# Performance work log

Measured on AMD Instinct MI355X. Metric: run time of the kernel, lower is better.

Reference implementation:

```python
import jax, jax.numpy as jnp
import numpy as np

D_MODEL = 1024
N_HEADS = 16
D_FF = 4096
EPS = 1e-5


def setup_inputs() -> dict:
    key = jax.random.key(0)
    ks = jax.random.split(key, 10)
    sig_attn = (1.0 / D_MODEL) ** 0.5
    sig1 = (2.0 / (D_MODEL + D_FF)) ** 0.5
    sig2 = (2.0 / (D_FF + D_MODEL)) ** 0.5
    return {
        "x": jax.random.normal(ks[0], (4, 2048, D_MODEL), dtype=jnp.float32),
        "W_q": jax.random.normal(ks[1], (D_MODEL, D_MODEL), jnp.float32) * sig_attn,
        "W_k": jax.random.normal(ks[2], (D_MODEL, D_MODEL), jnp.float32) * sig_attn,
        "W_v": jax.random.normal(ks[3], (D_MODEL, D_MODEL), jnp.float32) * sig_attn,
        "W_o": jax.random.normal(ks[4], (D_MODEL, D_MODEL), jnp.float32) * sig_attn,
        "gamma1": jnp.ones((D_MODEL,), jnp.float32),
        "gamma2": jnp.ones((D_MODEL,), jnp.float32),
        "W1": jax.random.normal(ks[5], (D_FF, D_MODEL), jnp.float32) * sig1,  # gate proj
        "W2": jax.random.normal(ks[6], (D_MODEL, D_FF), jnp.float32) * sig2,  # down proj
        "W3": jax.random.normal(ks[7], (D_FF, D_MODEL), jnp.float32) * sig1,  # up proj
    }


def _rmsnorm(x, gamma, eps=EPS):
    # computed in fp32 as in the original, cast back to input dtype
    in_dtype = x.dtype
    xf = x.astype(jnp.float32)
    norm = jnp.sqrt(jnp.mean(xf * xf, axis=-1, keepdims=True) + eps)
    return ((xf / norm) * gamma).astype(in_dtype)


def _mha(x, W_q, W_k, W_v, W_o, n_heads=N_HEADS):
    B, S, D = x.shape
    d_h = D // n_heads
    # projections: weights stored as [d_out, d_in]
    q = jnp.einsum('bsd,ed->bse', x, W_q).reshape(B, S, n_heads, d_h).transpose(0, 2, 1, 3)
    k = jnp.einsum('bsd,ed->bse', x, W_k).reshape(B, S, n_heads, d_h).transpose(0, 2, 1, 3)
    v = jnp.einsum('bsd,ed->bse', x, W_v).reshape(B, S, n_heads, d_h).transpose(0, 2, 1, 3)
    scores = jnp.einsum('bhqd,bhkd->bhqk', q, k) / jnp.sqrt(jnp.asarray(d_h, x.dtype))
    causal = jnp.tril(jnp.ones((S, S), dtype=bool))  # True = keep
    scores = jnp.where(causal, scores, -jnp.inf)
    probs = jax.nn.softmax(scores, axis=-1)
    out = jnp.einsum('bhqk,bhkd->bhqd', probs, v)
    out = out.transpose(0, 2, 1, 3).reshape(B, S, D)
    return jnp.einsum('bse,de->bsd', out, W_o)


def _swiglu(x, W1, W2, W3):
    g = jnp.einsum('bsd,fd->bsf', x, W1)
    u = jnp.einsum('bsd,fd->bsf', x, W3)
    return jnp.einsum('bsf,df->bsd', jax.nn.silu(g) * u, W2)


def reference(x, W_q, W_k, W_v, W_o, gamma1, gamma2, W1, W2, W3):
    x = x + _mha(_rmsnorm(x, gamma1), W_q, W_k, W_v, W_o)
    x = x + _swiglu(_rmsnorm(x, gamma2), W1, W2, W3)
    return x
```

## Files before the change

### kernel.cpp

```cpp
#include <hip/hip_runtime.h>
#include <cstdint>
#include <cstddef>

typedef unsigned short u16;
typedef unsigned int u32;
typedef short bf16x8 __attribute__((ext_vector_type(8)));
typedef float f32x4 __attribute__((ext_vector_type(4)));
typedef float f32x16 __attribute__((ext_vector_type(16)));
typedef u16 u16x4 __attribute__((ext_vector_type(4)));

__device__ __forceinline__ u16 f2bf(float f) {
  u32 u = __float_as_uint(f);
  return (u16)((u + 0x7FFFu + ((u >> 16) & 1u)) >> 16);
}
__device__ __forceinline__ float bf2f(u16 h) {
  return __uint_as_float(((u32)h) << 16);
}
__device__ __forceinline__ u32 pack2(float a, float b) {
  return (u32)f2bf(a) | ((u32)f2bf(b) << 16);
}

__device__ __forceinline__ void gload_lds16(const void* g, void* l) {
  __builtin_amdgcn_global_load_lds((const __attribute__((address_space(1))) u32*)g,
                                   (__attribute__((address_space(3))) u32*)l, 16, 0, 0);
}

__global__ __launch_bounds__(256) void castw(const float* __restrict__ src,
                                             u16* __restrict__ dst, int n4) {
  int i = blockIdx.x * 256 + threadIdx.x;
  if (i < n4) {
    float4 v = ((const float4*)src)[i];
    u16x4 r;
    r.x = f2bf(v.x); r.y = f2bf(v.y); r.z = f2bf(v.z); r.w = f2bf(v.w);
    ((u16x4*)dst)[i] = r;
  }
}

__global__ __launch_bounds__(256) void rmsnorm_k(const float* __restrict__ x,
                                                 const float* __restrict__ gamma,
                                                 u16* __restrict__ o) {
  const int row = blockIdx.x;
  const int t = threadIdx.x;
  float4 v = ((const float4*)(x + (size_t)row * 1024))[t];
  float ss = v.x * v.x + v.y * v.y + v.z * v.z + v.w * v.w;
  #pragma unroll
  for (int m = 1; m < 64; m <<= 1) ss += __shfl_xor(ss, m);
  __shared__ float wsum[4];
  if ((t & 63) == 0) wsum[t >> 6] = ss;
  __syncthreads();
  float tot = wsum[0] + wsum[1] + wsum[2] + wsum[3];
  float inv = rsqrtf(tot * (1.0f / 1024.0f) + 1e-5f);
  float4 g = ((const float4*)gamma)[t];
  u16x4 r;
  r.x = f2bf(v.x * inv * g.x);
  r.y = f2bf(v.y * inv * g.y);
  r.z = f2bf(v.z * inv * g.z);
  r.w = f2bf(v.w * inv * g.w);
  ((u16x4*)(o + (size_t)row * 1024))[t] = r;
}

template <int EPI>
__global__ __launch_bounds__(256, 4)
void gemm128(const u16* __restrict__ A, const u16* __restrict__ B,
             void* out, const void* ep, int M, int N, int KLOOP, int KS,
             float scale, int ncut) {
  __shared__ u16 smem[2][8192];
  u16* const sA = smem[0];
  u16* const sB = smem[1];

  const int tid = threadIdx.x;
  const int lane = tid & 63;
  const int w = tid >> 6;
  const int wr = w >> 1, wc = w & 1;
  const int lr = lane & 15, lk = lane >> 4;

  A += (size_t)blockIdx.z * KLOOP;
  B += (size_t)blockIdx.z * KLOOP;

  const int nx = gridDim.x;
  const int nwg = nx * gridDim.y;
  const int flat = blockIdx.y * nx + blockIdx.x;
  const int qq = nwg >> 3, rr = nwg & 7;
  const int xcd = flat & 7, off = flat >> 3;
  const int swz = (xcd < rr ? xcd * (qq + 1) : rr * (qq + 1) + (xcd - rr) * qq) + off;
  const int sr = nx * 8;
  const int g8 = swz / sr, rem = swz % sr;
  const int m0 = (g8 * 8 + (rem & 7)) * 128;
  const int n0 = (rem >> 3) * 128;

  f32x4 acc[4][4];
  #pragma unroll
  for (int i = 0; i < 4; i++)
    #pragma unroll
    for (int j = 0; j < 4; j++) acc[i][j] = (f32x4){0.f, 0.f, 0.f, 0.f};

  for (int kt = 0; kt < KLOOP; kt += 64) {
    __syncthreads();
    #pragma unroll
    for (int r = 0; r < 4; r++) {
      const int q = r * 256 + tid;
      const int row = q >> 3;
      const int cs = (q & 7) ^ (row & 7);
      gload_lds16(A + (size_t)(m0 + row) * KS + kt + cs * 8, (char*)sA + q * 16);
      gload_lds16(B + (size_t)(n0 + row) * KS + kt + cs * 8, (char*)sB + q * 16);
    }
    __syncthreads();
    #pragma unroll
    for (int kk = 0; kk < 2; kk++) {
      bf16x8 a_[4], b_[4];
      #pragma unroll
      for (int i = 0; i < 4; i++)
        a_[i] = *(const bf16x8*)&sA[(wr * 64 + i * 16 + lr) * 64 +
                                    (((kk * 4 + lk) ^ (lr & 7)) * 8)];
      #pragma unroll
      for (int j = 0; j < 4; j++)
        b_[j] = *(const bf16x8*)&sB[(wc * 64 + j * 16 + lr) * 64 +
                                    (((kk * 4 + lk) ^ (lr & 7)) * 8)];
      #pragma unroll
      for (int i = 0; i < 4; i++)
        #pragma unroll
        for (int j = 0; j < 4; j++)
          acc[i][j] = __builtin_amdgcn_mfma_f32_16x16x32_bf16(a_[i], b_[j], acc[i][j], 0, 0, 0);
    }
  }

  if constexpr (EPI == 1 || EPI == 3) {
    #pragma unroll
    for (int i = 0; i < 4; i++)
      #pragma unroll
      for (int j = 0; j < 4; j++)
        #pragma unroll
        for (int r = 0; r < 4; r++) {
          const int grow = m0 + wr * 64 + i * 16 + lk * 4 + r;
          const int gcol = n0 + wc * 64 + j * 16 + lr;
          const size_t idx = (size_t)grow * N + gcol;
          if (EPI == 1) ((float*)out)[idx] = ((const float*)ep)[idx] + acc[i][j][r];
          else          unsafeAtomicAdd((float*)out + idx, acc[i][j][r]);
        }
  } else {
    u16* const smC = smem[0];
    const float s = (EPI == 0 && n0 < ncut) ? scale : 1.0f;
    __syncthreads();
    #pragma unroll
    for (int i = 0; i < 4; i++)
      #pragma unroll
      for (int j = 0; j < 4; j++)
        #pragma unroll
        for (int r = 0; r < 4; r++) {
          const int row = wr * 64 + i * 16 + lk * 4 + r;
          const int col = wc * 64 + j * 16 + lr;
          smC[row * 128 + (col ^ ((row & 7) << 3))] = f2bf(acc[i][j][r] * s);
        }
    __syncthreads();
    #pragma unroll
    for (int it = 0; it < 8; it++) {
      const int fl = it * 256 + tid;
      const int row = fl >> 4;
      const int ch = fl & 15;
      bf16x8 cv = *(const bf16x8*)&smC[row * 128 + ((ch ^ (row & 7)) * 8)];
      const size_t gidx = (size_t)(m0 + row) * N + n0 + ch * 8;
      if (EPI == 0) {
        *(bf16x8*)((u16*)out + gidx) = cv;
      } else {
        bf16x8 gv = *(const bf16x8*)((const u16*)ep + gidx);
        bf16x8 ov;
        #pragma unroll
        for (int k = 0; k < 8; k++) {
          float g = bf2f((u16)gv[k]);
          float sg = g / (1.f + __expf(-g));
          ov[k] = (short)f2bf(sg * bf2f((u16)cv[k]));
        }
        *(bf16x8*)((u16*)out + gidx) = ov;
      }
    }
  }
}

__global__ __launch_bounds__(256) void vtrans(const u16* __restrict__ qkv,
                                              u16* __restrict__ vt) {
  __shared__ u16 T[64][72];
  const int t = threadIdx.x;
  const int s0 = blockIdx.x * 64;
  const int h = blockIdx.y;
  const int b = blockIdx.z;
  const int sl = t >> 2, dl = (t & 3) * 16;
  const u16* src = qkv + ((size_t)(b * 2048 + s0 + sl)) * 3072 + 2048 + h * 64 + dl;
  bf16x8 v0 = *(const bf16x8*)src;
  bf16x8 v1 = *(const bf16x8*)(src + 8);
  #pragma unroll
  for (int j = 0; j < 8; j++) T[dl + j][sl] = (u16)v0[j];
  #pragma unroll
  for (int j = 0; j < 8; j++) T[dl + 8 + j][sl] = (u16)v1[j];
  __syncthreads();
  const int dl2 = t >> 2, sl2 = (t & 3) * 16;
  u16* dst = vt + ((size_t)((b * 16 + h) * 64 + dl2)) * 2048 + s0 + sl2;
  *(bf16x8*)dst = *(const bf16x8*)&T[dl2][sl2];
  *(bf16x8*)(dst + 8) = *(const bf16x8*)&T[dl2][sl2 + 8];
}

__global__ __launch_bounds__(256)
void attn_fwd2(const u16* __restrict__ qkv, const u16* __restrict__ vt,
               u16* __restrict__ o) {
  __shared__ u16 sm[9216];
  u16* const smK = sm;
  u16* const smV = sm + 4096;

  const int tid = threadIdx.x;
  const int lane = tid & 63;
  const int w = tid >> 6;
  const int hi = lane >> 5;
  const int ln = lane & 31;

  const int flat = blockIdx.y * 16 + blockIdx.x;
  const int swz = (flat & 7) * 128 + (flat >> 3);
  const int qt = swz & 15;
  const int bh = swz >> 4;
  const int b = bh >> 4, h = bh & 15;

  const int qbase = qt * 128;
  const int qw0 = qbase + w * 32;
  const int qglob = qw0 + ln;
  const int nkb = qt * 2 + 2;

  bf16x8 qf[4];
  {
    const u16* qp = qkv + ((size_t)(b * 2048 + qw0 + ln)) * 3072 + h * 64 + hi * 8;
    #pragma unroll
    for (int c = 0; c < 4; c++) qf[c] = *(const bf16x8*)(qp + c * 16);
  }

  f32x16 accO[2];
  #pragma unroll
  for (int i = 0; i < 2; i++)
    #pragma unroll
    for (int r = 0; r < 16; r++) accO[i][r] = 0.f;
  float mrun = -1e30f, lsum = 0.f;

  for (int kb = 0; kb < nkb; kb++) {
    const int kbase = kb * 64;
    __syncthreads();
    #pragma unroll
    for (int r = 0; r < 2; r++) {
      const int cb = w * 128 + r * 64;
      const int ci = cb + lane;
      {
        const int key = ci >> 3, gch = (ci & 7) ^ (key & 7);
        const u16* src = qkv + ((size_t)(b * 2048 + kbase + key)) * 3072 + 1024 + h * 64 + gch * 8;
        gload_lds16(src, (char*)smK + cb * 16);
      }
      {
        const int d = ci >> 3, gch = (ci & 7) ^ (d & 7);
        const u16* src = vt + ((size_t)(bh * 64 + d)) * 2048 + kbase + gch * 8;
        gload_lds16(src, (char*)smV + cb * 16);
      }
    }
    __syncthreads();

    if (kbase <= qw0 + 31) {
      f32x16 st[2];
      #pragma unroll
      for (int kt = 0; kt < 2; kt++) {
        #pragma unroll
        for (int r = 0; r < 16; r++) st[kt][r] = 0.f;
        #pragma unroll
        for (int c = 0; c < 4; c++) {
          const int row = kt * 32 + ln;
          const int sch = (c * 2 + hi) ^ (ln & 7);
          bf16x8 kf = *(const bf16x8*)((const char*)smK + row * 128 + sch * 16);
          st[kt] = __builtin_amdgcn_mfma_f32_32x32x16_bf16(kf, qf[c], st[kt], 0, 0, 0);
        }
      }
      if (kbase + 63 > qw0) {
        #pragma unroll
        for (int kt = 0; kt < 2; kt++)
          #pragma unroll
          for (int r = 0; r < 16; r++) {
            const int kk = kbase + kt * 32 + (r & 3) + 8 * (r >> 2) + 4 * hi;
            if (kk > qglob) st[kt][r] = -1e30f;
          }
      }
      float pm = st[0][0];
      #pragma unroll
      for (int kt = 0; kt < 2; kt++)
        #pragma unroll
        for (int r = 0; r < 16; r++) pm = fmaxf(pm, st[kt][r]);
      pm = fmaxf(pm, __shfl_xor(pm, 32));
      const float mnew = fmaxf(mrun, pm);
      const float alpha = __expf(mrun - mnew);
      float ps = 0.f;
      #pragma unroll
      for (int kt = 0; kt < 2; kt++)
        #pragma unroll
        for (int r = 0; r < 16; r++) {
          const float p = __expf(st[kt][r] - mnew);
          st[kt][r] = p;
          ps += p;
        }
      ps += __shfl_xor(ps, 32);
      lsum = lsum * alpha + ps;
      mrun = mnew;
      accO[0] *= alpha;
      accO[1] *= alpha;

      #pragma unroll
      for (int kt = 0; kt < 2; kt++) {
        u32 pw[8], px[8];
        #pragma unroll
        for (int i = 0; i < 8; i++) pw[i] = pack2(st[kt][2 * i], st[kt][2 * i + 1]);
        #pragma unroll
        for (int i = 0; i < 8; i++) px[i] = (u32)__shfl_xor((int)pw[i], 32);
        union { u32 wd[4]; bf16x8 v; } f0, f1;
        f0.wd[0] = hi ? px[2] : pw[0];
        f0.wd[1] = hi ? px[3] : pw[1];
        f0.wd[2] = hi ? pw[2] : px[0];
        f0.wd[3] = hi ? pw[3] : px[1];
        f1.wd[0] = hi ? px[6] : pw[4];
        f1.wd[1] = hi ? px[7] : pw[5];
        f1.wd[2] = hi ? pw[6] : px[4];
        f1.wd[3] = hi ? pw[7] : px[5];
        #pragma unroll
        for (int d0 = 0; d0 < 2; d0++) {
          #pragma unroll
          for (int kc = 0; kc < 2; kc++) {
            const int drow = d0 * 32 + ln;
            const int sch = (kt * 4 + kc * 2 + hi) ^ (ln & 7);
            bf16x8 vf = *(const bf16x8*)((const char*)smV + drow * 128 + sch * 16);
            accO[d0] = __builtin_amdgcn_mfma_f32_32x32x16_bf16(vf, kc ? f1.v : f0.v,
                                                               accO[d0], 0, 0, 0);
          }
        }
      }
    }
  }

  __syncthreads();
  const float inv = 1.0f / lsum;
  #pragma unroll
  for (int d0 = 0; d0 < 2; d0++)
    #pragma unroll
    for (int r = 0; r < 16; r++) {
      const int d = d0 * 32 + (r & 3) + 8 * (r >> 2) + 4 * hi;
      sm[(w * 32 + ln) * 72 + d] = f2bf(accO[d0][r] * inv);
    }
  __syncthreads();
  const int ql = tid >> 1, dh = (tid & 1) * 32;
  const u16* srcp = &sm[ql * 72 + dh];
  u16* dst = o + ((size_t)(b * 2048 + qbase + ql)) * 1024 + h * 64 + dh;
  #pragma unroll
  for (int j = 0; j < 4; j++)
    *(bf16x8*)(dst + j * 8) = *(const bf16x8*)(srcp + j * 8);
}

extern "C" void kernel_launch(void* const* d_in, const int* in_sizes, int n_in,
                              void* d_out, int out_size, void* d_ws, size_t ws_size,
                              hipStream_t stream) {
  const float* x      = (const float*)d_in[0];
  const float* W_q    = (const float*)d_in[1];
  const float* W_k    = (const float*)d_in[2];
  const float* W_v    = (const float*)d_in[3];
  const float* W_o    = (const float*)d_in[4];
  const float* gamma1 = (const float*)d_in[5];
  const float* gamma2 = (const float*)d_in[6];
  const float* W1     = (const float*)d_in[7];
  const float* W2     = (const float*)d_in[8];
  const float* W3     = (const float*)d_in[9];

  char* ws = (char*)d_ws;
  const size_t MB = 1ull << 20;
  u16* qkvw  = (u16*)(ws + 0 * MB);
  u16* Wo_b  = (u16*)(ws + 6 * MB);
  u16* W1_b  = (u16*)(ws + 8 * MB);
  u16* W3_b  = (u16*)(ws + 16 * MB);
  u16* W2_b  = (u16*)(ws + 24 * MB);
  u16* xn    = (u16*)(ws + 32 * MB);
  u16* qkvb  = (u16*)(ws + 48 * MB);
  u16* attnb = (u16*)(ws + 96 * MB);
  u16* vtb   = (u16*)(ws + 112 * MB);
  u16* gbuf  = (u16*)(ws + 112 * MB);
  u16* hbuf  = (u16*)(ws + 48 * MB);
  float* x1  = (float*)d_out;

  castw<<<1024, 256, 0, stream>>>(W_q, qkvw, 262144);
  castw<<<1024, 256, 0, stream>>>(W_k, qkvw + 1024 * 1024, 262144);
  castw<<<1024, 256, 0, stream>>>(W_v, qkvw + 2048 * 1024, 262144);
  castw<<<1024, 256, 0, stream>>>(W_o, Wo_b, 262144);
  castw<<<4096, 256, 0, stream>>>(W1, W1_b, 1048576);
  castw<<<4096, 256, 0, stream>>>(W3, W3_b, 1048576);
  castw<<<4096, 256, 0, stream>>>(W2, W2_b, 1048576);

  rmsnorm_k<<<8192, 256, 0, stream>>>(x, gamma1, xn);
  gemm128<0><<<dim3(24, 64), 256, 0, stream>>>(xn, qkvw, qkvb, nullptr,
                                               8192, 3072, 1024, 1024, 0.125f, 1024);
  vtrans<<<dim3(32, 16, 4), 256, 0, stream>>>(qkvb, vtb);
  attn_fwd2<<<dim3(16, 64), 256, 0, stream>>>(qkvb, vtb, attnb);
  gemm128<1><<<dim3(8, 64), 256, 0, stream>>>(attnb, Wo_b, x1, x,
                                              8192, 1024, 1024, 1024, 1.0f, 0);

  rmsnorm_k<<<8192, 256, 0, stream>>>(x1, gamma2, xn);
  gemm128<0><<<dim3(32, 64), 256, 0, stream>>>(xn, W1_b, gbuf, nullptr,
                                               8192, 4096, 1024, 1024, 1.0f, 0);
  gemm128<2><<<dim3(32, 64), 256, 0, stream>>>(xn, W3_b, hbuf, gbuf,
                                               8192, 4096, 1024, 1024, 1.0f, 0);
  gemm128<3><<<dim3(8, 64, 2), 256, 0, stream>>>(hbuf, W2_b, (float*)d_out, nullptr,
                                                 8192, 1024, 2048, 4096, 1.0f, 0);
}
```

Measured before the change: 522.0 us.

## Pair causal query tiles per block and streamline attention softmax with exp2

```diff
diff --git a/kernel.cpp b/kernel.cpp
--- a/kernel.cpp
+++ b/kernel.cpp
@@ -16,8 +16,15 @@
 __device__ __forceinline__ float bf2f(u16 h) {
   return __uint_as_float(((u32)h) << 16);
 }
-__device__ __forceinline__ u32 pack2(float a, float b) {
-  return (u32)f2bf(a) | ((u32)f2bf(b) << 16);
+__device__ __forceinline__ u32 cvtpk(float lo, float hi) {
+  u32 r;
+  asm("v_cvt_pk_bf16_f32 %0, %1, %2" : "=v"(r) : "v"(lo), "v"(hi));
+  return r;
+}
+__device__ __forceinline__ float exp2a(float x) {
+  float r;
+  asm("v_exp_f32 %0, %1" : "=v"(r) : "v"(x));
+  return r;
 }
 
 __device__ __forceinline__ void gload_lds16(const void* g, void* l) {
@@ -198,8 +205,8 @@
   *(bf16x8*)(dst + 8) = *(const bf16x8*)&T[dl2][sl2 + 8];
 }
 
-__global__ __launch_bounds__(256)
-void attn_fwd2(const u16* __restrict__ qkv, const u16* __restrict__ vt,
+__global__ __launch_bounds__(256, 2)
+void attn_fwd3(const u16* __restrict__ qkv, const u16* __restrict__ vt,
                u16* __restrict__ o) {
   __shared__ u16 sm[9216];
   u16* const smK = sm;
@@ -211,144 +218,164 @@
   const int hi = lane >> 5;
   const int ln = lane & 31;
 
-  const int flat = blockIdx.y * 16 + blockIdx.x;
-  const int swz = (flat & 7) * 128 + (flat >> 3);
-  const int qt = swz & 15;
-  const int bh = swz >> 4;
+  const int bh = blockIdx.x;
+  const int pair = blockIdx.y;
   const int b = bh >> 4, h = bh & 15;
 
-  const int qbase = qt * 128;
-  const int qw0 = qbase + w * 32;
-  const int qglob = qw0 + ln;
-  const int nkb = qt * 2 + 2;
-
-  bf16x8 qf[4];
-  {
-    const u16* qp = qkv + ((size_t)(b * 2048 + qw0 + ln)) * 3072 + h * 64 + hi * 8;
-    #pragma unroll
-    for (int c = 0; c < 4; c++) qf[c] = *(const bf16x8*)(qp + c * 16);
-  }
-
-  f32x16 accO[2];
-  #pragma unroll
-  for (int i = 0; i < 2; i++)
-    #pragma unroll
-    for (int r = 0; r < 16; r++) accO[i][r] = 0.f;
-  float mrun = -1e30f, lsum = 0.f;
-
-  for (int kb = 0; kb < nkb; kb++) {
-    const int kbase = kb * 64;
-    __syncthreads();
-    #pragma unroll
-    for (int r = 0; r < 2; r++) {
-      const int cb = w * 128 + r * 64;
-      const int ci = cb + lane;
-      {
-        const int key = ci >> 3, gch = (ci & 7) ^ (key & 7);
-        const u16* src = qkv + ((size_t)(b * 2048 + kbase + key)) * 3072 + 1024 + h * 64 + gch * 8;
-        gload_lds16(src, (char*)smK + cb * 16);
+  #pragma unroll 1
+  for (int phase = 0; phase < 2; ++phase) {
+    const int qt = phase ? (15 - pair) : pair;
+    const int qbase = qt * 128;
+    const int qw0 = qbase + w * 32;
+    const int qglob = qw0 + ln;
+    const int nkb = qt * 2 + 2;
+
+    bf16x8 qf[4];
+    {
+      const u16* qp = qkv + ((size_t)(b * 2048 + qw0 + ln)) * 3072 + h * 64 + hi * 8;
+      #pragma unroll
+      for (int c = 0; c < 4; c++) qf[c] = *(const bf16x8*)(qp + c * 16);
+    }
+
+    f32x16 accO[2];
+    #pragma unroll
+    for (int i = 0; i < 2; i++)
+      #pragma unroll
+      for (int r = 0; r < 16; r++) accO[i][r] = 0.f;
+    float mrun = -1e30f, lsum = 0.f;
+
+    for (int kb = 0; kb < nkb; kb++) {
+      const int kbase = kb * 64;
+      __syncthreads();
+      #pragma unroll
+      for (int r = 0; r < 2; r++) {
+        const int cb = w * 128 + r * 64;
+        const int ci = cb + lane;
+        {
+          const int key = ci >> 3, gch = (ci & 7) ^ (key & 7);
+          const u16* src = qkv + ((size_t)(b * 2048 + kbase + key)) * 3072 + 1024 + h * 64 + gch * 8;
+          gload_lds16(src, (char*)smK + cb * 16);
+        }
+        {
+          const int d = ci >> 3, gch = (ci & 7) ^ (d & 7);
+          const u16* src = vt + ((size_t)(bh * 64 + d)) * 2048 + kbase + gch * 8;
+          gload_lds16(src, (char*)smV + cb * 16);
+        }
       }
-      {
-        const int d = ci >> 3, gch = (ci & 7) ^ (d & 7);
-        const u16* src = vt + ((size_t)(bh * 64 + d)) * 2048 + kbase + gch * 8;
-        gload_lds16(src, (char*)smV + cb * 16);
+      __syncthreads();
+
+      if (kbase <= qw0 + 31) {
+        f32x16 st[2];
+        #pragma unroll
+        for (int kt = 0; kt < 2; kt++) {
+          #pragma unroll
+          for (int r = 0; r < 16; r++) st[kt][r] = 0.f;
+        }
+        __builtin_amdgcn_s_setprio(1);
+        #pragma unroll
+        for (int kt = 0; kt < 2; kt++)
+          #pragma unroll
+          for (int c = 0; c < 4; c++) {
+            const int row = kt * 32 + ln;
+            const int sch = (c * 2 + hi) ^ (ln & 7);
+            bf16x8 kf = *(const bf16x8*)((const char*)smK + row * 128 + sch * 16);
+            st[kt] = __builtin_amdgcn_mfma_f32_32x32x16_bf16(kf, qf[c], st[kt], 0, 0, 0);
+          }
+        __builtin_amdgcn_s_setprio(0);
+        if (kbase + 63 > qw0) {
+          #pragma unroll
+          for (int kt = 0; kt < 2; kt++)
+            #pragma unroll
+            for (int r = 0; r < 16; r++) {
+              const int kk = kbase + kt * 32 + (r & 3) + 8 * (r >> 2) + 4 * hi;
+              if (kk > qglob) st[kt][r] = -1e30f;
+            }
+        }
+        float t16[16];
+        #pragma unroll
+        for (int i = 0; i < 16; i++) t16[i] = fmaxf(st[0][i], st[1][i]);
+        #pragma unroll
+        for (int s = 8; s > 0; s >>= 1)
+          #pragma unroll
+          for (int i = 0; i < 8; i++)
+            if (i < s) t16[i] = fmaxf(t16[i], t16[i + s]);
+        float pm = t16[0];
+        pm = fmaxf(pm, __shfl_xor(pm, 32));
+        if (!__all(pm - mrun <= 8.f)) {
+          const float mnew = fmaxf(mrun, pm);
+          const float alpha = exp2a(mrun - mnew);
+          lsum *= alpha;
+          accO[0] *= alpha;
+          accO[1] *= alpha;
+          mrun = mnew;
+        }
+        #pragma unroll
+        for (int kt = 0; kt < 2; kt++)
+          #pragma unroll
+          for (int r = 0; r < 16; r++) st[kt][r] = exp2a(st[kt][r] - mrun);
+        float s16[16];
+        #pragma unroll
+        for (int i = 0; i < 16; i++) s16[i] = st[0][i] + st[1][i];
+        #pragma unroll
+        for (int s = 8; s > 0; s >>= 1)
+          #pragma unroll
+          for (int i = 0; i < 8; i++)
+            if (i < s) s16[i] = s16[i] + s16[i + s];
+        float ps = s16[0];
+        ps += __shfl_xor(ps, 32);
+        lsum += ps;
+
+        #pragma unroll
+        for (int kt = 0; kt < 2; kt++) {
+          u32 pw[8], px[8];
+          #pragma unroll
+          for (int i = 0; i < 8; i++) pw[i] = cvtpk(st[kt][2 * i], st[kt][2 * i + 1]);
+          #pragma unroll
+          for (int i = 0; i < 8; i++) px[i] = (u32)__shfl_xor((int)pw[i], 32);
+          union { u32 wd[4]; bf16x8 v; } f0, f1;
+          f0.wd[0] = hi ? px[2] : pw[0];
+          f0.wd[1] = hi ? px[3] : pw[1];
+          f0.wd[2] = hi ? pw[2] : px[0];
+          f0.wd[3] = hi ? pw[3] : px[1];
+          f1.wd[0] = hi ? px[6] : pw[4];
+          f1.wd[1] = hi ? px[7] : pw[5];
+          f1.wd[2] = hi ? pw[6] : px[4];
+          f1.wd[3] = hi ? pw[7] : px[5];
+          __builtin_amdgcn_s_setprio(1);
+          #pragma unroll
+          for (int d0 = 0; d0 < 2; d0++) {
+            #pragma unroll
+            for (int kc = 0; kc < 2; kc++) {
+              const int drow = d0 * 32 + ln;
+              const int sch = (kt * 4 + kc * 2 + hi) ^ (ln & 7);
+              bf16x8 vf = *(const bf16x8*)((const char*)smV + drow * 128 + sch * 16);
+              accO[d0] = __builtin_amdgcn_mfma_f32_32x32x16_bf16(vf, kc ? f1.v : f0.v,
+                                                                 accO[d0], 0, 0, 0);
+            }
+          }
+          __builtin_amdgcn_s_setprio(0);
+        }
       }
     }
-    __syncthreads();
-
-    if (kbase <= qw0 + 31) {
-      f32x16 st[2];
-      #pragma unroll
-      for (int kt = 0; kt < 2; kt++) {
-        #pragma unroll
-        for (int r = 0; r < 16; r++) st[kt][r] = 0.f;
-        #pragma unroll
-        for (int c = 0; c < 4; c++) {
-          const int row = kt * 32 + ln;
-          const int sch = (c * 2 + hi) ^ (ln & 7);
-          bf16x8 kf = *(const bf16x8*)((const char*)smK + row * 128 + sch * 16);
-          st[kt] = __builtin_amdgcn_mfma_f32_32x32x16_bf16(kf, qf[c], st[kt], 0, 0, 0);
-        }
+
+    __syncthreads();
+    const float inv = 1.0f / lsum;
+    #pragma unroll
+    for (int d0 = 0; d0 < 2; d0++)
+      #pragma unroll
+      for (int r = 0; r < 16; r++) {
+        const int d = d0 * 32 + (r & 3) + 8 * (r >> 2) + 4 * hi;
+        sm[(w * 32 + ln) * 72 + d] = f2bf(accO[d0][r] * inv);
       }
-      if (kbase + 63 > qw0) {
-        #pragma unroll
-        for (int kt = 0; kt < 2; kt++)
-          #pragma unroll
-          for (int r = 0; r < 16; r++) {
-            const int kk = kbase + kt * 32 + (r & 3) + 8 * (r >> 2) + 4 * hi;
-            if (kk > qglob) st[kt][r] = -1e30f;
-          }
-      }
-      float pm = st[0][0];
-      #pragma unroll
-      for (int kt = 0; kt < 2; kt++)
-        #pragma unroll
-        for (int r = 0; r < 16; r++) pm = fmaxf(pm, st[kt][r]);
-      pm = fmaxf(pm, __shfl_xor(pm, 32));
-      const float mnew = fmaxf(mrun, pm);
-      const float alpha = __expf(mrun - mnew);
-      float ps = 0.f;
-      #pragma unroll
-      for (int kt = 0; kt < 2; kt++)
-        #pragma unroll
-        for (int r = 0; r < 16; r++) {
-          const float p = __expf(st[kt][r] - mnew);
-          st[kt][r] = p;
-          ps += p;
-        }
-      ps += __shfl_xor(ps, 32);
-      lsum = lsum * alpha + ps;
-      mrun = mnew;
-      accO[0] *= alpha;
-      accO[1] *= alpha;
-
-      #pragma unroll
-      for (int kt = 0; kt < 2; kt++) {
-        u32 pw[8], px[8];
-        #pragma unroll
-        for (int i = 0; i < 8; i++) pw[i] = pack2(st[kt][2 * i], st[kt][2 * i + 1]);
-        #pragma unroll
-        for (int i = 0; i < 8; i++) px[i] = (u32)__shfl_xor((int)pw[i], 32);
-        union { u32 wd[4]; bf16x8 v; } f0, f1;
-        f0.wd[0] = hi ? px[2] : pw[0];
-        f0.wd[1] = hi ? px[3] : pw[1];
-        f0.wd[2] = hi ? pw[2] : px[0];
-        f0.wd[3] = hi ? pw[3] : px[1];
-        f1.wd[0] = hi ? px[6] : pw[4];
-        f1.wd[1] = hi ? px[7] : pw[5];
-        f1.wd[2] = hi ? pw[6] : px[4];
-        f1.wd[3] = hi ? pw[7] : px[5];
-        #pragma unroll
-        for (int d0 = 0; d0 < 2; d0++) {
-          #pragma unroll
-          for (int kc = 0; kc < 2; kc++) {
-            const int drow = d0 * 32 + ln;
-            const int sch = (kt * 4 + kc * 2 + hi) ^ (ln & 7);
-            bf16x8 vf = *(const bf16x8*)((const char*)smV + drow * 128 + sch * 16);
-            accO[d0] = __builtin_amdgcn_mfma_f32_32x32x16_bf16(vf, kc ? f1.v : f0.v,
-                                                               accO[d0], 0, 0, 0);
-          }
-        }
-      }
-    }
+    __syncthreads();
+    const int ql = tid >> 1, dh = (tid & 1) * 32;
+    const u16* srcp = &sm[ql * 72 + dh];
+    u16* dst = o + ((size_t)(b * 2048 + qbase + ql)) * 1024 + h * 64 + dh;
+    #pragma unroll
+    for (int j = 0; j < 4; j++)
+      *(bf16x8*)(dst + j * 8) = *(const bf16x8*)(srcp + j * 8);
+    __syncthreads();
   }
-
-  __syncthreads();
-  const float inv = 1.0f / lsum;
-  #pragma unroll
-  for (int d0 = 0; d0 < 2; d0++)
-    #pragma unroll
-    for (int r = 0; r < 16; r++) {
-      const int d = d0 * 32 + (r & 3) + 8 * (r >> 2) + 4 * hi;
-      sm[(w * 32 + ln) * 72 + d] = f2bf(accO[d0][r] * inv);
-    }
-  __syncthreads();
-  const int ql = tid >> 1, dh = (tid & 1) * 32;
-  const u16* srcp = &sm[ql * 72 + dh];
-  u16* dst = o + ((size_t)(b * 2048 + qbase + ql)) * 1024 + h * 64 + dh;
-  #pragma unroll
-  for (int j = 0; j < 4; j++)
-    *(bf16x8*)(dst + j * 8) = *(const bf16x8*)(srcp + j * 8);
 }
 
 extern "C" void kernel_launch(void* const* d_in, const int* in_sizes, int n_in,
@@ -390,9 +417,10 @@
 
   rmsnorm_k<<<8192, 256, 0, stream>>>(x, gamma1, xn);
   gemm128<0><<<dim3(24, 64), 256, 0, stream>>>(xn, qkvw, qkvb, nullptr,
-                                               8192, 3072, 1024, 1024, 0.125f, 1024);
+                                               8192, 3072, 1024, 1024,
+                                               0.125f * 1.44269504f, 1024);
   vtrans<<<dim3(32, 16, 4), 256, 0, stream>>>(qkvb, vtb);
-  attn_fwd2<<<dim3(16, 64), 256, 0, stream>>>(qkvb, vtb, attnb);
+  attn_fwd3<<<dim3(64, 8), 256, 0, stream>>>(qkvb, vtb, attnb);
   gemm128<1><<<dim3(8, 64), 256, 0, stream>>>(attnb, Wo_b, x1, x,
                                               8192, 1024, 1024, 1024, 1.0f, 0);
 
```

After: 489.5 us. 1.07x faster.
